# Kernel tuning notes

Hardware: AMD Instinct MI355X
Metric: run time of the kernel (lower is better)

Reference implementation:

```python
import jax, jax.numpy as jnp
import numpy as np

B, T, S = 64, 19, 80          # batch, decoder steps (max_length_targ-1), memory length (max_length_inp)
V, E, U = 32000, 256, 1024    # vocab, embedding_dim, dec_units


def setup_inputs() -> dict:
    key = jax.random.key(0)
    ks = jax.random.split(key, 12)
    s = 0.02
    return {
        "x": jax.random.randint(ks[0], (B, T), 0, V, dtype=jnp.int32),
        "enc_state": jax.random.normal(ks[1], (B, U), jnp.float32),
        "memory": jax.random.normal(ks[2], (B, S, U), jnp.float32),
        "embedding": jax.random.normal(ks[3], (V, E), jnp.float32) * s,
        "gru_kernel": jax.random.normal(ks[4], (E + U, 3 * U), jnp.float32) * s,
        "gru_rec_kernel": jax.random.normal(ks[5], (U, 3 * U), jnp.float32) * s,
        "gru_bias": jnp.zeros((2, 3 * U), jnp.float32),  # [input_bias, recurrent_bias] (reset_after=True)
        "mem_W": jax.random.normal(ks[6], (U, U), jnp.float32) * s,   # Luong memory layer (no bias)
        "attn_W": jax.random.normal(ks[7], (2 * U, U), jnp.float32) * s,  # attention layer (no bias)
        "fc_W": jax.random.normal(ks[8], (U, V), jnp.float32) * s,
        "fc_b": jnp.zeros((V,), jnp.float32),
    }


def _decode(x, enc_state, memory, embedding, gru_kernel, gru_rec_kernel,
            gru_bias, mem_W, attn_W, fc_W, fc_b):
    # Precompute Luong keys: memory_layer(memory)  -> [B,S,U]
    keys = jnp.einsum("bsu,uv->bsv", memory, mem_W)
    b_in, b_rec = gru_bias[0], gru_bias[1]

    def step(carry, x_t):
        h, attn_prev = carry                       # [B,U], [B,U]
        e = embedding[x_t]                         # [B,E]
        cell_in = jnp.concatenate([e, attn_prev], axis=-1)  # [B,E+U]
        # Keras GRUCell, reset_after=True, gate order [z, r, h]
        xm = cell_in @ gru_kernel + b_in           # [B,3U]
        hm = h @ gru_rec_kernel + b_rec            # [B,3U]
        z = jax.nn.sigmoid(xm[:, :U] + hm[:, :U])
        r = jax.nn.sigmoid(xm[:, U:2 * U] + hm[:, U:2 * U])
        hh = jnp.tanh(xm[:, 2 * U:] + r * hm[:, 2 * U:])
        h_new = z * h + (1.0 - z) * hh             # [B,U]
        # Luong attention: score = query . keys (all S positions valid: lengths = S)
        score = jnp.einsum("bu,bsu->bs", h_new, keys)      # [B,S]
        align = jax.nn.softmax(score, axis=-1)
        context = jnp.einsum("bs,bsu->bu", align, memory)  # [B,U]
        attn = jnp.concatenate([h_new, context], axis=-1) @ attn_W  # [B,U]
        logits = attn @ fc_W + fc_b                # [B,V]
        return (h_new, attn), logits

    init = (enc_state, jnp.zeros((B, U), enc_state.dtype))
    _, logits = jax.lax.scan(step, init, jnp.transpose(x))  # xs: [T,B]
    return jnp.transpose(logits, (1, 0, 2))        # [B,T,V] (batch-major rnn_output)


def reference(x, enc_state, memory, embedding, gru_kernel, gru_rec_kernel,
              gru_bias, mem_W, attn_W, fc_W, fc_b):
    return _decode(x, enc_state, memory, embedding, gru_kernel, gru_rec_kernel,
                   gru_bias, mem_W, attn_W, fc_W, fc_b)
```

## Files before the change

kernel.cpp:

```cpp
#include <hip/hip_runtime.h>
#include <hip/hip_bf16.h>
#include <math.h>

#define B 64
#define T 19
#define S 80
#define V 32000
#define E 256
#define U 1024
#define U3 (3*U)
#define KXM (E+U)

typedef unsigned short ushortT;
typedef __attribute__((ext_vector_type(8))) __bf16 bf16x8;
typedef __attribute__((ext_vector_type(4))) float f32x4;

__device__ __forceinline__ ushortT f2bf(float f) {
    unsigned int u = __float_as_uint(f);
    u = (u + 0x7FFF + ((u >> 16) & 1)) >> 16;
    return (ushortT)u;
}
__device__ __forceinline__ float bf2f(ushortT u) {
    return __uint_as_float(((unsigned int)u) << 16);
}
__device__ __forceinline__ void split3(float v, ushortT& hi, ushortT& mid, ushortT& lo) {
    hi = f2bf(v);
    float r1 = v - bf2f(hi);
    mid = f2bf(r1);
    float r2 = r1 - bf2f(mid);
    lo = f2bf(r2);
}

struct PackJob { const float* W; ushortT* Wp; int N; int K; int blk0; };

__global__ __launch_bounds__(256) void pack_w3_all(
    PackJob j0, PackJob j1, PackJob j2, PackJob j3, PackJob j4)
{
    int bid = blockIdx.x;
    PackJob J = j4;
    if (bid < j1.blk0) J = j0;
    else if (bid < j2.blk0) J = j1;
    else if (bid < j3.blk0) J = j2;
    else if (bid < j4.blk0) J = j3;

    int idx = (bid - J.blk0) * 256 + threadIdx.x;
    int lane = idx & 63;
    int t = idx >> 6;
    int KC = J.K >> 5;
    int ntile = t / KC, kc = t - ntile * KC;
    int col = ntile * 16 + (lane & 15);
    int krow = kc * 32 + (lane >> 4) * 8;
    ushortT hi[8], mi[8], lo[8];
    #pragma unroll
    for (int i = 0; i < 8; i++)
        split3(J.W[(size_t)(krow + i) * J.N + col], hi[i], mi[i], lo[i]);
    size_t ps = (size_t)J.K * J.N;
    *(uint4*)(J.Wp + (size_t)idx * 8)          = *(uint4*)hi;
    *(uint4*)(J.Wp + ps + (size_t)idx * 8)     = *(uint4*)mi;
    *(uint4*)(J.Wp + 2 * ps + (size_t)idx * 8) = *(uint4*)lo;
}

__global__ __launch_bounds__(256) void pack_w(
    const float* __restrict__ W, ushortT* __restrict__ Wp, int N, int K)
{
    int idx = blockIdx.x * 256 + threadIdx.x;
    int lane = idx & 63;
    int t = idx >> 6;
    int KC = K >> 5;
    int ntile = t / KC, kc = t - ntile * KC;
    int col = ntile * 16 + (lane & 15);
    int krow = kc * 32 + (lane >> 4) * 8;
    ushortT tmp[8];
    #pragma unroll
    for (int i = 0; i < 8; i++)
        tmp[i] = f2bf(W[(size_t)(krow + i) * N + col]);
    *(uint4*)(Wp + (size_t)idx * 8) = *(uint4*)tmp;
}

struct GemmJob {
    const float*   A;
    const float*   W;
    const ushortT* Wp;
    unsigned long long ps;
    int kc_base;
    int KCtot;
    float* Cpart;
    int lda;
};

template<bool PRESPLIT>
__device__ __forceinline__ void gemm6_body(
    const GemmJob& J, int xblk, int ks, int nkc, int N,
    ushortT* Ahi, ushortT* Amid, ushortT* Alo)
{
    const int tid = threadIdx.x;
    const int lane = tid & 63;
    const int wave = tid >> 6;
    const int ntile = xblk * 4 + wave;
    const int col = ntile * 16 + (lane & 15);
    const int kfrag = (lane >> 4) * 8;

    f32x4 acc[4] = {};
    const int arow = (tid >> 6) * 16 + (tid & 15);
    const int kgof = ((tid >> 4) & 3) * 8;

    for (int c = 0; c < nkc; c++) {
        const int kc = ks * nkc + c;
        const float* ar = J.A + (size_t)arow * J.lda + kc * 32 + kgof;
        float av[8];
        *(float4*)(av)     = *(const float4*)(ar);
        *(float4*)(av + 4) = *(const float4*)(ar + 4);
        ushortT thi[8], tmi[8], tlo[8];
        #pragma unroll
        for (int i = 0; i < 8; i++) split3(av[i], thi[i], tmi[i], tlo[i]);
        ((uint4*)Ahi)[tid]  = *(const uint4*)thi;
        ((uint4*)Amid)[tid] = *(const uint4*)tmi;
        ((uint4*)Alo)[tid]  = *(const uint4*)tlo;

        bf16x8 bh, bm, bl;
        if constexpr (PRESPLIT) {
            size_t fi = (((size_t)ntile * J.KCtot + (J.kc_base + kc)) * 64 + lane) * 8;
            bh = *(const bf16x8*)(J.Wp + fi);
            bm = *(const bf16x8*)(J.Wp + J.ps + fi);
            bl = *(const bf16x8*)(J.Wp + 2 * J.ps + fi);
        } else {
            const float* wp = J.W + (size_t)((J.kc_base + kc) * 32 + kfrag) * N + col;
            ushortT whi[8], wmi[8], wlo[8];
            #pragma unroll
            for (int i = 0; i < 8; i++)
                split3(wp[(size_t)i * N], whi[i], wmi[i], wlo[i]);
            bh = *(const bf16x8*)whi;
            bm = *(const bf16x8*)wmi;
            bl = *(const bf16x8*)wlo;
        }

        __syncthreads();
        #pragma unroll
        for (int mi = 0; mi < 4; mi++) {
            bf16x8 ah = *(const bf16x8*)(Ahi  + (mi * 64 + lane) * 8);
            bf16x8 am = *(const bf16x8*)(Amid + (mi * 64 + lane) * 8);
            bf16x8 al = *(const bf16x8*)(Alo  + (mi * 64 + lane) * 8);
            acc[mi] = __builtin_amdgcn_mfma_f32_16x16x32_bf16(ah, bh, acc[mi], 0, 0, 0);
            acc[mi] = __builtin_amdgcn_mfma_f32_16x16x32_bf16(am, bh, acc[mi], 0, 0, 0);
            acc[mi] = __builtin_amdgcn_mfma_f32_16x16x32_bf16(ah, bm, acc[mi], 0, 0, 0);
            acc[mi] = __builtin_amdgcn_mfma_f32_16x16x32_bf16(am, bm, acc[mi], 0, 0, 0);
            acc[mi] = __builtin_amdgcn_mfma_f32_16x16x32_bf16(al, bh, acc[mi], 0, 0, 0);
            acc[mi] = __builtin_amdgcn_mfma_f32_16x16x32_bf16(ah, bl, acc[mi], 0, 0, 0);
        }
        __syncthreads();
    }

    float* cp = J.Cpart + (size_t)ks * 64 * N;
    #pragma unroll
    for (int mi = 0; mi < 4; mi++) {
        #pragma unroll
        for (int r = 0; r < 4; r++) {
            int m = mi * 16 + (lane >> 4) * 4 + r;
            cp[(size_t)m * N + col] = acc[mi][r];
        }
    }
}

template<bool PRESPLIT>
__global__ __launch_bounds__(256) void gemm6_ks2(
    GemmJob j0, GemmJob j1, int N, int nkc)
{
    __shared__ __align__(16) ushortT Ahi[2048];
    __shared__ __align__(16) ushortT Amid[2048];
    __shared__ __align__(16) ushortT Alo[2048];
    const GemmJob J = blockIdx.z ? j1 : j0;
    gemm6_body<PRESPLIT>(J, blockIdx.x, blockIdx.y, nkc, N, Ahi, Amid, Alo);
}

template<bool PRESPLIT>
__global__ __launch_bounds__(256) void gemm_keys(
    const float* __restrict__ A, const float* __restrict__ W,
    const ushortT* __restrict__ Wp, float* __restrict__ C)
{
    const int tid = threadIdx.x;
    const int lane = tid & 63;
    const int wave = tid >> 6;
    const int row0 = blockIdx.y * 64;
    const int nt0 = blockIdx.x * 8 + wave * 2;
    const int col0 = nt0 * 16 + (lane & 15);
    const int kfrag = (lane >> 4) * 8;

    __shared__ __align__(16) ushortT Ahi[2048];
    __shared__ __align__(16) ushortT Amid[2048];
    __shared__ __align__(16) ushortT Alo[2048];

    f32x4 acc[2][4] = {};
    const int arow = row0 + (tid >> 6) * 16 + (tid & 15);
    const int kgof = ((tid >> 4) & 3) * 8;
    const size_t ps = (size_t)U * U;

    for (int kc = 0; kc < 32; kc++) {
        const float* ar = A + (size_t)arow * U + kc * 32 + kgof;
        float av[8];
        *(float4*)(av)     = *(const float4*)(ar);
        *(float4*)(av + 4) = *(const float4*)(ar + 4);
        ushortT thi[8], tmi[8], tlo[8];
        #pragma unroll
        for (int i = 0; i < 8; i++) split3(av[i], thi[i], tmi[i], tlo[i]);
        ((uint4*)Ahi)[tid]  = *(const uint4*)thi;
        ((uint4*)Amid)[tid] = *(const uint4*)tmi;
        ((uint4*)Alo)[tid]  = *(const uint4*)tlo;

        bf16x8 bh[2], bm[2], bl[2];
        #pragma unroll
        for (int j = 0; j < 2; j++) {
            if constexpr (PRESPLIT) {
                size_t fi = (((size_t)(nt0 + j) * 32 + kc) * 64 + lane) * 8;
                bh[j] = *(const bf16x8*)(Wp + fi);
                bm[j] = *(const bf16x8*)(Wp + ps + fi);
                bl[j] = *(const bf16x8*)(Wp + 2 * ps + fi);
            } else {
                const float* wp = W + (size_t)(kc * 32 + kfrag) * U + col0 + j * 16;
                ushortT whi[8], wmi[8], wlo[8];
                #pragma unroll
                for (int i = 0; i < 8; i++)
                    split3(wp[(size_t)i * U], whi[i], wmi[i], wlo[i]);
                bh[j] = *(const bf16x8*)whi;
                bm[j] = *(const bf16x8*)wmi;
                bl[j] = *(const bf16x8*)wlo;
            }
        }

        __syncthreads();
        #pragma unroll
        for (int mi = 0; mi < 4; mi++) {
            bf16x8 ah = *(const bf16x8*)(Ahi  + (mi * 64 + lane) * 8);
            bf16x8 am = *(const bf16x8*)(Amid + (mi * 64 + lane) * 8);
            bf16x8 al = *(const bf16x8*)(Alo  + (mi * 64 + lane) * 8);
            #pragma unroll
            for (int j = 0; j < 2; j++) {
                acc[j][mi] = __builtin_amdgcn_mfma_f32_16x16x32_bf16(ah, bh[j], acc[j][mi], 0, 0, 0);
                acc[j][mi] = __builtin_amdgcn_mfma_f32_16x16x32_bf16(am, bh[j], acc[j][mi], 0, 0, 0);
                acc[j][mi] = __builtin_amdgcn_mfma_f32_16x16x32_bf16(ah, bm[j], acc[j][mi], 0, 0, 0);
                acc[j][mi] = __builtin_amdgcn_mfma_f32_16x16x32_bf16(am, bm[j], acc[j][mi], 0, 0, 0);
                acc[j][mi] = __builtin_amdgcn_mfma_f32_16x16x32_bf16(al, bh[j], acc[j][mi], 0, 0, 0);
                acc[j][mi] = __builtin_amdgcn_mfma_f32_16x16x32_bf16(ah, bl[j], acc[j][mi], 0, 0, 0);
            }
        }
        __syncthreads();
    }

    #pragma unroll
    for (int mi = 0; mi < 4; mi++) {
        #pragma unroll
        for (int r = 0; r < 4; r++) {
            int m = row0 + mi * 16 + (lane >> 4) * 4 + r;
            #pragma unroll
            for (int j = 0; j < 2; j++)
                C[(size_t)m * U + col0 + j * 16] = acc[j][mi][r];
        }
    }
}

template<bool PRESPLIT>
__global__ __launch_bounds__(256) void gemm_xe(
    const int* __restrict__ x, const float* __restrict__ emb,
    const float* __restrict__ gk, const ushortT* __restrict__ gkp,
    float* __restrict__ xe)
{
    const int tid = threadIdx.x;
    const int lane = tid & 63;
    const int wave = tid >> 6;
    const int t = blockIdx.y;
    const int ntile = blockIdx.x * 4 + wave;
    const int col = ntile * 16 + (lane & 15);
    const int kfrag = (lane >> 4) * 8;

    __shared__ __align__(16) ushortT Ahi[2048];
    __shared__ __align__(16) ushortT Amid[2048];
    __shared__ __align__(16) ushortT Alo[2048];

    f32x4 acc[4] = {};
    const int b = (tid >> 6) * 16 + (tid & 15);
    const int tok = x[b * T + t];
    const int kgof = ((tid >> 4) & 3) * 8;
    const size_t ps = (size_t)KXM * U3;

    for (int kc = 0; kc < E / 32; kc++) {
        const float* ar = emb + (size_t)tok * E + kc * 32 + kgof;
        float av[8];
        *(float4*)(av)     = *(const float4*)(ar);
        *(float4*)(av + 4) = *(const float4*)(ar + 4);
        ushortT thi[8], tmi[8], tlo[8];
        #pragma unroll
        for (int i = 0; i < 8; i++) split3(av[i], thi[i], tmi[i], tlo[i]);
        ((uint4*)Ahi)[tid]  = *(const uint4*)thi;
        ((uint4*)Amid)[tid] = *(const uint4*)tmi;
        ((uint4*)Alo)[tid]  = *(const uint4*)tlo;

        bf16x8 bh, bm, bl;
        if constexpr (PRESPLIT) {
            size_t fi = (((size_t)ntile * 40 + kc) * 64 + lane) * 8;
            bh = *(const bf16x8*)(gkp + fi);
            bm = *(const bf16x8*)(gkp + ps + fi);
            bl = *(const bf16x8*)(gkp + 2 * ps + fi);
        } else {
            const float* wp = gk + (size_t)(kc * 32 + kfrag) * U3 + col;
            ushortT whi[8], wmi[8], wlo[8];
            #pragma unroll
            for (int i = 0; i < 8; i++)
                split3(wp[(size_t)i * U3], whi[i], wmi[i], wlo[i]);
            bh = *(const bf16x8*)whi;
            bm = *(const bf16x8*)wmi;
            bl = *(const bf16x8*)wlo;
        }

        __syncthreads();
        #pragma unroll
        for (int mi = 0; mi < 4; mi++) {
            bf16x8 ah = *(const bf16x8*)(Ahi  + (mi * 64 + lane) * 8);
            bf16x8 am = *(const bf16x8*)(Amid + (mi * 64 + lane) * 8);
            bf16x8 al = *(const bf16x8*)(Alo  + (mi * 64 + lane) * 8);
            acc[mi] = __builtin_amdgcn_mfma_f32_16x16x32_bf16(ah, bh, acc[mi], 0, 0, 0);
            acc[mi] = __builtin_amdgcn_mfma_f32_16x16x32_bf16(am, bh, acc[mi], 0, 0, 0);
            acc[mi] = __builtin_amdgcn_mfma_f32_16x16x32_bf16(ah, bm, acc[mi], 0, 0, 0);
            acc[mi] = __builtin_amdgcn_mfma_f32_16x16x32_bf16(am, bm, acc[mi], 0, 0, 0);
            acc[mi] = __builtin_amdgcn_mfma_f32_16x16x32_bf16(al, bh, acc[mi], 0, 0, 0);
            acc[mi] = __builtin_amdgcn_mfma_f32_16x16x32_bf16(ah, bl, acc[mi], 0, 0, 0);
        }
        __syncthreads();
    }

    #pragma unroll
    for (int mi = 0; mi < 4; mi++) {
        #pragma unroll
        for (int r = 0; r < 4; r++) {
            int m = mi * 16 + (lane >> 4) * 4 + r;
            xe[((size_t)t * 64 + m) * U3 + col] = acc[mi][r];
        }
    }
}

__global__ __launch_bounds__(256) void gemm_fcB(
    const ushortT* __restrict__ A, const ushortT* __restrict__ Wp,
    const float* __restrict__ bias, float* __restrict__ C)
{
    const int xcd = blockIdx.x & 7;
    const int rem = blockIdx.x >> 3;
    const int g = rem / T;
    const int tg = rem - g * T;
    const int strip = g * 8 + xcd;
    if (strip >= V / 128) return;

    const int tid = threadIdx.x;
    const int lane = tid & 63;
    const int wave = tid >> 6;
    const int nt0 = strip * 8 + wave * 2;
    const int col0 = nt0 * 16 + (lane & 15);

    __shared__ __align__(16) ushortT As[2][2048];

    f32x4 acc[2][4] = {};
    const int arow = (tid >> 6) * 16 + (tid & 15);
    const ushortT* At = A + (size_t)tg * 64 * U;
    float* Ct = C + (size_t)tg * V;
    const int kgof = ((tid >> 4) & 3) * 8;

    for (int it = 0; it < 16; it++) {
        #pragma unroll
        for (int c = 0; c < 2; c++) {
            const ushortT* ar = At + (size_t)arow * U + (it * 2 + c) * 32 + kgof;
            ((uint4*)As[c])[tid] = *(const uint4*)ar;
        }
        bf16x8 b[2][2];
        #pragma unroll
        for (int c = 0; c < 2; c++)
            #pragma unroll
            for (int j = 0; j < 2; j++)
                b[c][j] = *(const bf16x8*)(Wp +
                    (((size_t)(nt0 + j) * 32 + it * 2 + c) * 64 + lane) * 8);
        __syncthreads();
        #pragma unroll
        for (int c = 0; c < 2; c++) {
            #pragma unroll
            for (int mi = 0; mi < 4; mi++) {
                bf16x8 a = *(const bf16x8*)(As[c] + (mi * 64 + lane) * 8);
                #pragma unroll
                for (int j = 0; j < 2; j++)
                    acc[j][mi] = __builtin_amdgcn_mfma_f32_16x16x32_bf16(a, b[c][j], acc[j][mi], 0, 0, 0);
            }
        }
        __syncthreads();
    }

    #pragma unroll
    for (int j = 0; j < 2; j++) {
        const float bv = bias[col0 + j * 16];
        #pragma unroll
        for (int mi = 0; mi < 4; mi++) {
            #pragma unroll
            for (int r = 0; r < 4; r++) {
                int m = mi * 16 + (lane >> 4) * 4 + r;
                __builtin_nontemporal_store(acc[j][mi][r] + bv,
                    &Ct[(size_t)m * (T * V) + col0 + j * 16]);
            }
        }
    }
}

__global__ __launch_bounds__(256) void gates_k(
    const float* __restrict__ xe_t, const float* __restrict__ xm_part,
    const float* __restrict__ hm_part, const float* __restrict__ gb,
    float* __restrict__ h, int use_xm)
{
    int idx = blockIdx.x * 256 + threadIdx.x;
    int b = idx >> 10, u = idx & (U - 1);
    float xv[3], hv[3];
    #pragma unroll
    for (int g = 0; g < 3; g++) {
        int j = g * U + u;
        float xs = xe_t[(size_t)b * U3 + j] + gb[j];
        float hsum = gb[U3 + j];
        if (use_xm) {
            #pragma unroll
            for (int p = 0; p < 8; p++)
                xs += xm_part[((size_t)p * 64 + b) * U3 + j];
        }
        #pragma unroll
        for (int p = 0; p < 8; p++)
            hsum += hm_part[((size_t)p * 64 + b) * U3 + j];
        xv[g] = xs; hv[g] = hsum;
    }
    float z = 1.f / (1.f + expf(-(xv[0] + hv[0])));
    float r = 1.f / (1.f + expf(-(xv[1] + hv[1])));
    float hh = tanhf(xv[2] + r * hv[2]);
    h[idx] = z * h[idx] + (1.f - z) * hh;
}

template<bool PRESPLIT>
__global__ __launch_bounds__(256) void sc_ah(
    const float* __restrict__ h, const float* __restrict__ keys,
    float* __restrict__ scores,
    const float* __restrict__ Wtop, const ushortT* __restrict__ wtpp,
    float* __restrict__ ah_part)
{
    __shared__ __align__(16) ushortT Ahi[2048];
    __shared__ __align__(16) ushortT Amid[2048];
    __shared__ __align__(16) ushortT Alo[2048];

    const int bid = blockIdx.x;
    if (bid < B * S / 4) {
        int gw = bid * 4 + (threadIdx.x >> 6);
        int lane = threadIdx.x & 63;
        int b = gw / S, s = gw - b * S;
        const float* kr = keys + ((size_t)b * S + s) * U;
        const float* hr = h + (size_t)b * U;
        float acc = 0.f;
        #pragma unroll
        for (int c = 0; c < 4; c++) {
            int off = c * 256 + lane * 4;
            float4 kv = *(const float4*)(kr + off);
            float4 hv = *(const float4*)(hr + off);
            acc += kv.x * hv.x + kv.y * hv.y + kv.z * hv.z + kv.w * hv.w;
        }
        #pragma unroll
        for (int off = 32; off > 0; off >>= 1) acc += __shfl_down(acc, off);
        if (lane == 0) scores[gw] = acc;
    } else {
        int r = bid - B * S / 4;
        GemmJob job = { h, Wtop, wtpp, (size_t)U * U, 0, 32, ah_part, U };
        gemm6_body<PRESPLIT>(job, r & 15, r >> 4, 4, U, Ahi, Amid, Alo);
    }
}

__global__ __launch_bounds__(256) void pnmv_sm(
    const float* __restrict__ ah_part, const float* __restrict__ scores,
    const float* __restrict__ memV, float* __restrict__ dst,
    ushortT* __restrict__ dst_bf)
{
    const int b = blockIdx.x;
    const int u = blockIdx.y * 256 + threadIdx.x;
    __shared__ float p[S];
    __shared__ float pl[S];
    if (threadIdx.x < S) p[threadIdx.x] = scores[b * S + threadIdx.x];
    __syncthreads();
    float m = -1e30f;
    #pragma unroll 8
    for (int s = 0; s < S; s++) m = fmaxf(m, p[s]);
    float sum = 0.f;
    #pragma unroll 8
    for (int s = 0; s < S; s++) sum += expf(p[s] - m);
    if (threadIdx.x < S) pl[threadIdx.x] = expf(p[threadIdx.x] - m) / sum;
    __syncthreads();
    float acc = 0.f;
    #pragma unroll
    for (int pp = 0; pp < 8; pp++)
        acc += ah_part[((size_t)pp * 64 + b) * U + u];
    #pragma unroll 8
    for (int s = 0; s < S; s++)
        acc += pl[s] * memV[((size_t)b * S + s) * U + u];
    dst[(size_t)b * U + u] = acc;
    dst_bf[(size_t)b * U + u] = f2bf(acc);
}

extern "C" void kernel_launch(void* const* d_in, const int* in_sizes, int n_in,
                              void* d_out, int out_size, void* d_ws, size_t ws_size,
                              hipStream_t stream)
{
    const int*   x      = (const int*)  d_in[0];
    const float* enc    = (const float*)d_in[1];
    const float* memory = (const float*)d_in[2];
    const float* emb    = (const float*)d_in[3];
    const float* gk     = (const float*)d_in[4];
    const float* grk    = (const float*)d_in[5];
    const float* gb     = (const float*)d_in[6];
    const float* memW   = (const float*)d_in[7];
    const float* attnW  = (const float*)d_in[8];
    const float* fcW    = (const float*)d_in[9];
    const float* fcb    = (const float*)d_in[10];
    float* out = (float*)d_out;

    const float* Wtop = attnW;
    const float* Wbot = attnW + (size_t)U * U;

    char* p = (char*)d_ws;
    auto alloc = [&](size_t bytes) { char* r = p; p += (bytes + 255) & ~(size_t)255; return r; };
    ushortT* fcWp      = (ushortT*)alloc((size_t)U * V * 2);
    float*   keys      = (float*)  alloc((size_t)B * S * U * 4);
    float*   memV      = (float*)  alloc((size_t)B * S * U * 4);
    float*   xe        = (float*)  alloc((size_t)T * B * U3 * 4);
    float*   xm_part   = (float*)  alloc((size_t)8 * B * U3 * 4);
    float*   hm_part   = (float*)  alloc((size_t)8 * B * U3 * 4);
    float*   ah_part   = (float*)  alloc((size_t)8 * B * U * 4);
    float*   h         = (float*)  alloc((size_t)B * U * 4);
    float*   attnv_all = (float*)  alloc((size_t)T * B * U * 4);
    ushortT* attnv_bf  = (ushortT*)alloc((size_t)T * B * U * 2);
    float*   scores    = (float*)  alloc((size_t)B * S * 4);
    ushortT* gkp       = (ushortT*)alloc((size_t)KXM * U3 * 2 * 3);
    ushortT* grkp      = (ushortT*)alloc((size_t)U * U3 * 2 * 3);
    ushortT* wtpp      = (ushortT*)alloc((size_t)U * U * 2 * 3);
    ushortT* wbpp      = (ushortT*)alloc((size_t)U * U * 2 * 3);
    ushortT* mwp       = (ushortT*)alloc((size_t)U * U * 2 * 3);
    const bool PS = (size_t)(p - (char*)d_ws) <= ws_size;

    dim3 blk(256);

    if (PS) {
        PackJob j0 = { gk,   gkp,  U3, KXM, 0 };
        PackJob j1 = { grk,  grkp, U3, U,   1920 };
        PackJob j2 = { Wtop, wtpp, U,  U,   1920 + 1536 };
        PackJob j3 = { Wbot, wbpp, U,  U,   1920 + 1536 + 512 };
        PackJob j4 = { memW, mwp,  U,  U,   1920 + 1536 + 512 + 512 };
        pack_w3_all<<<1920 + 1536 + 512 + 512 + 512, blk, 0, stream>>>(j0, j1, j2, j3, j4);
    }
    pack_w<<<(size_t)U * V / 8 / 256, blk, 0, stream>>>(fcW, fcWp, V, U);
    (void)hipMemcpyAsync(h, enc, (size_t)B * U * sizeof(float),
                         hipMemcpyDeviceToDevice, stream);

    if (PS) gemm_xe<true><<<dim3(U3 / 64, T), blk, 0, stream>>>(x, emb, gk, gkp, xe);
    else    gemm_xe<false><<<dim3(U3 / 64, T), blk, 0, stream>>>(x, emb, gk, gkp, xe);

    if (PS) gemm_keys<true><<<dim3(U / 128, B * S / 64), blk, 0, stream>>>(memory, memW, mwp, keys);
    else    gemm_keys<false><<<dim3(U / 128, B * S / 64), blk, 0, stream>>>(memory, memW, mwp, keys);

    if (PS) gemm_keys<true><<<dim3(U / 128, B * S / 64), blk, 0, stream>>>(memory, Wbot, wbpp, memV);
    else    gemm_keys<false><<<dim3(U / 128, B * S / 64), blk, 0, stream>>>(memory, Wbot, wbpp, memV);

    GemmJob job_hm = { h, grk, grkp, (size_t)U * U3, 0, 32, hm_part, U };

    for (int t = 0; t < T; t++) {
        GemmJob job_xm = { attnv_all + (size_t)(t - 1) * B * U, gk, gkp,
                           (size_t)KXM * U3, 8, 40, xm_part, U };
        dim3 g1(U3 / 64, 8, t > 0 ? 2 : 1);
        if (PS) gemm6_ks2<true><<<g1, blk, 0, stream>>>(job_hm, job_xm, U3, 4);
        else    gemm6_ks2<false><<<g1, blk, 0, stream>>>(job_hm, job_xm, U3, 4);
        gates_k<<<B * U / 256, blk, 0, stream>>>(
            xe + (size_t)t * B * U3, xm_part, hm_part, gb, h, t > 0 ? 1 : 0);
        if (PS) sc_ah<true><<<B * S / 4 + 128, blk, 0, stream>>>(
            h, keys, scores, Wtop, wtpp, ah_part);
        else    sc_ah<false><<<B * S / 4 + 128, blk, 0, stream>>>(
            h, keys, scores, Wtop, wtpp, ah_part);
        pnmv_sm<<<dim3(B, U / 256), blk, 0, stream>>>(
            ah_part, scores, memV, attnv_all + (size_t)t * B * U,
            attnv_bf + (size_t)t * B * U);
    }

    gemm_fcB<<<32 * T * 8, blk, 0, stream>>>(attnv_bf, fcWp, fcb, out);
}
```

Baseline: 1.061 ms.

## Fuse next-step recurrent GEMM into scores/attention kernel to shorten the serial chain

Once h_new is known in step t, the h @ gru_rec_kernel GEMM for step t+1 is now computed inside the same launch as the attention scores and the h @ Wtop GEMM, as 384 extra blocks. The xm GEMM for the next step runs right after the attention output is produced. A single hm GEMM is issued before the loop for t=0. This moves the recurrent GEMM off the critical path and runs it alongside the score work, at the cost of a larger combined launch and a separate xm launch per step.

```diff
diff --git a/kernel.cpp b/kernel.cpp
--- a/kernel.cpp
+++ b/kernel.cpp
@@ -433,11 +433,13 @@
 }
 
 template<bool PRESPLIT>
-__global__ __launch_bounds__(256) void sc_ah(
+__global__ __launch_bounds__(256) void sc_ah_hm(
     const float* __restrict__ h, const float* __restrict__ keys,
     float* __restrict__ scores,
     const float* __restrict__ Wtop, const ushortT* __restrict__ wtpp,
-    float* __restrict__ ah_part)
+    float* __restrict__ ah_part,
+    const float* __restrict__ grk, const ushortT* __restrict__ grkp,
+    float* __restrict__ hm_part)
 {
     __shared__ __align__(16) ushortT Ahi[2048];
     __shared__ __align__(16) ushortT Amid[2048];
@@ -461,10 +463,14 @@
         #pragma unroll
         for (int off = 32; off > 0; off >>= 1) acc += __shfl_down(acc, off);
         if (lane == 0) scores[gw] = acc;
-    } else {
+    } else if (bid < B * S / 4 + 128) {
         int r = bid - B * S / 4;
         GemmJob job = { h, Wtop, wtpp, (size_t)U * U, 0, 32, ah_part, U };
         gemm6_body<PRESPLIT>(job, r & 15, r >> 4, 4, U, Ahi, Amid, Alo);
+    } else {
+        int r = bid - (B * S / 4 + 128);
+        GemmJob job = { h, grk, grkp, (size_t)U * U3, 0, 32, hm_part, U };
+        gemm6_body<PRESPLIT>(job, r % 48, r / 48, 4, U3, Ahi, Amid, Alo);
     }
 }
 
@@ -563,21 +569,26 @@
 
     GemmJob job_hm = { h, grk, grkp, (size_t)U * U3, 0, 32, hm_part, U };
 
+    if (PS) gemm6_ks2<true><<<dim3(U3 / 64, 8, 1), blk, 0, stream>>>(job_hm, job_hm, U3, 4);
+    else    gemm6_ks2<false><<<dim3(U3 / 64, 8, 1), blk, 0, stream>>>(job_hm, job_hm, U3, 4);
+
     for (int t = 0; t < T; t++) {
-        GemmJob job_xm = { attnv_all + (size_t)(t - 1) * B * U, gk, gkp,
-                           (size_t)KXM * U3, 8, 40, xm_part, U };
-        dim3 g1(U3 / 64, 8, t > 0 ? 2 : 1);
-        if (PS) gemm6_ks2<true><<<g1, blk, 0, stream>>>(job_hm, job_xm, U3, 4);
-        else    gemm6_ks2<false><<<g1, blk, 0, stream>>>(job_hm, job_xm, U3, 4);
         gates_k<<<B * U / 256, blk, 0, stream>>>(
             xe + (size_t)t * B * U3, xm_part, hm_part, gb, h, t > 0 ? 1 : 0);
-        if (PS) sc_ah<true><<<B * S / 4 + 128, blk, 0, stream>>>(
-            h, keys, scores, Wtop, wtpp, ah_part);
-        else    sc_ah<false><<<B * S / 4 + 128, blk, 0, stream>>>(
-            h, keys, scores, Wtop, wtpp, ah_part);
+        int nblk = B * S / 4 + 128 + (t < T - 1 ? 384 : 0);
+        if (PS) sc_ah_hm<true><<<nblk, blk, 0, stream>>>(
+            h, keys, scores, Wtop, wtpp, ah_part, grk, grkp, hm_part);
+        else    sc_ah_hm<false><<<nblk, blk, 0, stream>>>(
+            h, keys, scores, Wtop, wtpp, ah_part, grk, grkp, hm_part);
         pnmv_sm<<<dim3(B, U / 256), blk, 0, stream>>>(
             ah_part, scores, memV, attnv_all + (size_t)t * B * U,
             attnv_bf + (size_t)t * B * U);
+        if (t < T - 1) {
+            GemmJob job_xm = { attnv_all + (size_t)t * B * U, gk, gkp,
+                               (size_t)KXM * U3, 8, 40, xm_part, U };
+            if (PS) gemm6_ks2<true><<<dim3(U3 / 64, 8, 1), blk, 0, stream>>>(job_xm, job_xm, U3, 4);
+            else    gemm6_ks2<false><<<dim3(U3 / 64, 8, 1), blk, 0, stream>>>(job_xm, job_xm, U3, 4);
+        }
     }
 
     gemm_fcB<<<32 * T * 8, blk, 0, stream>>>(attnv_bf, fcWp, fcb, out);
```

Result: no change. 1.071 ms (+1.0%).
